# Performance work log

Hardware: AMD Instinct MI355X
Metric: run time of the kernel (lower is better)

## Reference

```python
import jax, jax.numpy as jnp
import numpy as np

N = 50000   # nodes
E = 600000  # edges
H = 128     # hidden_features
TW = 1      # time_window
L = 6       # hidden_layer
MSG_IN = 2 * H + TW + 2 + 1   # 260
UPD_IN = 2 * H + 1            # 257
LX = 1.0; LY = 1.0; TMAX = 1.0; DT = 0.01
EPS = 1e-5


def setup_inputs() -> dict:
    ks = iter(jax.random.split(jax.random.key(0), 64))
    rn = lambda s, sc=0.05: jax.random.normal(next(ks), s, dtype=jnp.float32) * sc
    z = lambda s: jnp.zeros(s, jnp.float32)
    o = lambda s: jnp.ones(s, jnp.float32)
    return {
        'u': rn((N, TW), 1.0),
        'pos': jax.random.uniform(next(ks), (N, 3), dtype=jnp.float32),
        'edge_index': jax.random.randint(next(ks), (2, E), 0, N),
        'emb_W1': rn((TW + 3, H)), 'emb_b1': z((H,)), 'emb_g1': o((H,)), 'emb_be1': z((H,)),
        'emb_W2': rn((H, H)), 'emb_b2': z((H,)), 'emb_g2': o((H,)), 'emb_be2': z((H,)),
        'm1_W': rn((L, MSG_IN, H)), 'm1_b': z((L, H)),
        'm2_W': rn((L, H, H)), 'm2_b': z((L, H)),
        'u1_W': rn((L, UPD_IN, H)), 'u1_b': z((L, H)),
        'u2_W': rn((L, H, H)), 'u2_b': z((L, H)),
        'bn_g': o((L, H)), 'bn_b': z((L, H)),
        'c1_W': rn((4, 1, 16)), 'c1_b': z((4,)),
        'c2_W': rn((8, 4, 12)), 'c2_b': z((8,)),
        'c3_W': rn((1, 8, 8)), 'c3_b': z((1,)),
    }


def _bn(x, g, b):
    # BatchNorm1d, training-mode batch statistics over node dim (biased var)
    mu = jnp.mean(x, 0)
    v = jnp.var(x, 0)
    return g * (x - mu) * jax.lax.rsqrt(v + EPS) + b


def _conv1d(x, W, b, stride):
    y = jax.lax.conv_general_dilated(x, W, (stride,), 'VALID',
                                     dimension_numbers=('NCH', 'OIH', 'NCH'))
    return y + b[None, :, None]


def _forward(u, pos, emb_W1, emb_b1, emb_g1, emb_be1, emb_W2, emb_b2, emb_g2, emb_be2,
             m1_W, m1_b, m2_W, m2_b, u1_W, u1_b, u2_W, u2_b, bn_g, bn_b,
             c1_W, c1_b, c2_W, c2_b, c3_W, c3_b, edge_index):
    px = pos[:, 1:2] / LX
    py = pos[:, 2:3] / LY
    variables = pos[:, 0:1] / TMAX  # pos_t, only eq variable

    # embedding MLP: Linear -> BN -> ReLU -> Linear -> BN
    h = jnp.concatenate([u, px, py, variables], -1) @ emb_W1 + emb_b1
    h = jax.nn.relu(_bn(h, emb_g1, emb_be1))
    h = _bn(h @ emb_W2 + emb_b2, emb_g2, emb_be2)

    src, dst = edge_index[0], edge_index[1]  # x_j = x[src], x_i = x[dst]
    du = u[dst] - u[src]
    dpx = px[dst] - px[src]
    dpy = py[dst] - py[src]
    var_i = variables[dst]
    deg = jax.ops.segment_sum(jnp.ones((E,), jnp.float32), dst, num_segments=N)
    deg = jnp.maximum(deg, 1.0)[:, None]  # mean aggregation denom (0-deg -> 0)

    for i in range(L):
        # message: cat(x_i, x_j, u_i-u_j, dpos_x, dpos_y, variables_i) -> 2xMLP
        msg_in = jnp.concatenate([h[dst], h[src], du, dpx, dpy, var_i], -1)  # [E,260]
        m = jax.nn.relu(msg_in @ m1_W[i] + m1_b[i])
        m = jax.nn.relu(m @ m2_W[i] + m2_b[i])
        agg = jax.ops.segment_sum(m, dst, num_segments=N) / deg  # mean scatter
        # update: cat(x, message, variables) -> 2xMLP, residual, BN
        up = jax.nn.relu(jnp.concatenate([h, agg, variables], -1) @ u1_W[i] + u1_b[i])
        up = jax.nn.relu(up @ u2_W[i] + u2_b[i])
        h = _bn(h + up, bn_g[i], bn_b[i])

    # output CNN over feature dim: [N,1,128] -> [N,1,1]
    x = h[:, None, :]
    x = jax.nn.relu(_conv1d(x, c1_W, c1_b, 3))
    x = jax.nn.relu(_conv1d(x, c2_W, c2_b, 3))
    diff = _conv1d(x, c3_W, c3_b, 2)[:, 0, :]  # [N, TW]

    dt = jnp.cumsum(jnp.full((1, TW), DT * 0.1, dtype=h.dtype), axis=1)
    return dt * diff


def reference(u, pos, edge_index, emb_W1, emb_b1, emb_g1, emb_be1, emb_W2, emb_b2,
              emb_g2, emb_be2, m1_W, m1_b, m2_W, m2_b, u1_W, u1_b, u2_W, u2_b,
              bn_g, bn_b, c1_W, c1_b, c2_W, c2_b, c3_W, c3_b):
    return _forward(u, pos, emb_W1, emb_b1, emb_g1, emb_be1, emb_W2, emb_b2, emb_g2,
                    emb_be2, m1_W, m1_b, m2_W, m2_b, u1_W, u1_b, u2_W, u2_b,
                    bn_g, bn_b, c1_W, c1_b, c2_W, c2_b, c3_W, c3_b, edge_index)
```

## Files before the change

kernel.cpp:

```cpp
#include <hip/hip_runtime.h>

#define NN 50000
#define NE 600000
#define HD 128
#define NL 6
#define DPB 16

typedef __attribute__((ext_vector_type(8))) short bf16x8;
typedef __attribute__((ext_vector_type(4))) float f32x4;

__device__ inline unsigned short f2bf(float x) {
  unsigned u = __float_as_uint(x);
  u += 0x7FFF + ((u >> 16) & 1);
  return (unsigned short)(u >> 16);
}
__device__ inline float bf2f(unsigned short s) {
  return __uint_as_float((unsigned)s << 16);
}
__device__ inline unsigned pk2(float a, float b) {
  return (unsigned)f2bf(a) | ((unsigned)f2bf(b) << 16);
}

__global__ void k_code(float* __restrict__ out, float code) {
  if (threadIdx.x == 0 && blockIdx.x == 0) out[0] = code;
}


__global__ __launch_bounds__(256) void k_w2t(const float* __restrict__ W, unsigned short* __restrict__ T) {
  int idx = blockIdx.x * 256 + threadIdx.x;
  if (idx >= NL * HD * HD) return;
  int l = idx >> 14, r = idx & 16383;
  int n = r >> 7, k = r & 127;
  T[idx] = f2bf(W[(l << 14) + (k << 7) + n]);
}

__global__ __launch_bounds__(256) void k_u1t(const float* __restrict__ W, unsigned short* __restrict__ T) {
  int idx = blockIdx.x * 256 + threadIdx.x;
  if (idx >= NL * 128 * 256) return;
  int l = idx >> 15, r = idx & 32767;
  int n = r >> 8, k = r & 255;
  T[idx] = f2bf(W[l * 32896 + k * 128 + n]);
}

__global__ __launch_bounds__(256) void k_abt(const float* __restrict__ W, unsigned short* __restrict__ T) {
  int idx = blockIdx.x * 256 + threadIdx.x;
  if (idx >= NL * 256 * 128) return;
  int l = idx >> 15, r = idx & 32767;
  int n = r >> 7, k = r & 127;
  int row = (n < 128) ? k : 128 + k;
  int col = n & 127;
  T[idx] = f2bf(W[l * 33280 + row * 128 + col]);
}


__global__ __launch_bounds__(256) void k_deg(const int* __restrict__ ei, int* __restrict__ deg) {
  int e = blockIdx.x * 256 + threadIdx.x;
  if (e < NE) {
    int d = ei[NE + e];
    if (d >= 0 && d < NN) atomicAdd(&deg[d], 1);
  }
}

__global__ __launch_bounds__(256) void k_scan1(const int* __restrict__ deg, int* __restrict__ cursor,
                                               int* __restrict__ blk, float* __restrict__ invd) {
  __shared__ int sd[256];
  int t = threadIdx.x;
  int i = blockIdx.x * 256 + t;
  int v = (i < NN) ? deg[i] : 0;
  sd[t] = v;
  __syncthreads();
  for (int off = 1; off < 256; off <<= 1) {
    int x = (t >= off) ? sd[t - off] : 0;
    __syncthreads();
    if (t >= off) sd[t] += x;
    __syncthreads();
  }
  int incl = sd[t];
  if (i < NN) {
    cursor[i] = incl - v;
    invd[i] = 1.0f / fmaxf((float)v, 1.0f);
  }
  if (t == 255) blk[blockIdx.x] = incl;
}

__global__ __launch_bounds__(256) void k_scan2(int* __restrict__ blk, int nb) {
  __shared__ int sd[256];
  int t = threadIdx.x;
  int v = (t < nb) ? blk[t] : 0;
  sd[t] = v;
  __syncthreads();
  for (int off = 1; off < 256; off <<= 1) {
    int x = (t >= off) ? sd[t - off] : 0;
    __syncthreads();
    if (t >= off) sd[t] += x;
    __syncthreads();
  }
  if (t < nb) blk[t] = sd[t] - v;
}

__global__ __launch_bounds__(256) void k_scan3(int* __restrict__ cursor, const int* __restrict__ blk,
                                               int* __restrict__ rowstart) {
  int i = blockIdx.x * 256 + threadIdx.x;
  if (i < NN) {
    int v = cursor[i] + blk[blockIdx.x];
    cursor[i] = v;
    rowstart[i] = v;
  }
  if (i == 0) rowstart[NN] = NE;
}

__global__ __launch_bounds__(256) void k_scatter(const int* __restrict__ ei, const float* __restrict__ u,
                                                 const float* __restrict__ pos, int* __restrict__ cursor,
                                                 int* __restrict__ ssrc, int* __restrict__ sdst,
                                                 float* __restrict__ sfeat) {
  int e = blockIdx.x * 256 + threadIdx.x;
  if (e >= NE) return;
  int s = ei[e], d = ei[NE + e];
  s = s < 0 ? 0 : (s >= NN ? NN - 1 : s);
  d = d < 0 ? 0 : (d >= NN ? NN - 1 : d);
  int p = atomicAdd(&cursor[d], 1);
  ssrc[p] = s;
  sdst[p] = d;
  float du  = u[d] - u[s];
  float dpx = pos[d*3+1] - pos[s*3+1];
  float dpy = pos[d*3+2] - pos[s*3+2];
  float vi  = pos[d*3+0];
  ((float4*)sfeat)[p] = make_float4(du, dpx, dpy, vi);
}


__global__ __launch_bounds__(256) void k_emb1(const float* __restrict__ u, const float* __restrict__ pos,
                                              const float* __restrict__ W, const float* __restrict__ b,
                                              float* __restrict__ h, double* __restrict__ P) {
  __shared__ float xs[32 * 129];
  int tid = threadIdx.x;
  int nl = tid & 31, jg = tid >> 5;
  int gn = blockIdx.x * 32 + nl;
  float f0 = 0.f, f1 = 0.f, f2 = 0.f, f3 = 0.f;
  if (gn < NN) { f0 = u[gn]; f1 = pos[gn*3+1]; f2 = pos[gn*3+2]; f3 = pos[gn*3+0]; }
  float x[16];
#pragma unroll
  for (int q = 0; q < 4; ++q) {
    int j = (jg << 4) + (q << 2);
    float4 w0 = *(const float4*)(W + 0*HD + j);
    float4 w1 = *(const float4*)(W + 1*HD + j);
    float4 w2 = *(const float4*)(W + 2*HD + j);
    float4 w3 = *(const float4*)(W + 3*HD + j);
    float4 bb = *(const float4*)(b + j);
    x[q*4+0] = f0*w0.x + f1*w1.x + f2*w2.x + f3*w3.x + bb.x;
    x[q*4+1] = f0*w0.y + f1*w1.y + f2*w2.y + f3*w3.y + bb.y;
    x[q*4+2] = f0*w0.z + f1*w1.z + f2*w2.z + f3*w3.z + bb.z;
    x[q*4+3] = f0*w0.w + f1*w1.w + f2*w2.w + f3*w3.w + bb.w;
  }
  if (gn < NN) {
#pragma unroll
    for (int q = 0; q < 4; ++q)
      *(float4*)(h + (size_t)gn*HD + (jg<<4) + (q<<2)) = make_float4(x[q*4+0], x[q*4+1], x[q*4+2], x[q*4+3]);
  }
#pragma unroll
  for (int i = 0; i < 16; ++i) xs[nl*129 + (jg<<4) + i] = (gn < NN) ? x[i] : 0.f;
  __syncthreads();
  if (tid < HD) {
    double s = 0.0, sq = 0.0;
    for (int e = 0; e < 32; ++e) { double v = (double)xs[e*129 + tid]; s += v; sq += v*v; }
    size_t pb = (size_t)blockIdx.x * 256;
    P[pb + tid] = s;
    P[pb + 128 + tid] = sq;
  }
}

__global__ __launch_bounds__(256) void k_emb2(float* __restrict__ h, const float* __restrict__ W,
                                              const float* __restrict__ b, double* __restrict__ P) {
  __shared__ float hs[32 * 129];
  int tid = threadIdx.x;
  int base = blockIdx.x * 32;
#pragma unroll
  for (int r = 0; r < 16; ++r) {
    int lin = r*256 + tid;
    int n = lin >> 7, j = lin & 127;
    int gn = base + n;
    hs[n*129 + j] = (gn < NN) ? h[(size_t)gn*HD + j] : 0.f;
  }
  __syncthreads();
  int nl = tid & 31, jg = tid >> 5;
  int gn = base + nl;
  float acc[16];
#pragma unroll
  for (int q = 0; q < 4; ++q) {
    float4 bb = *(const float4*)(b + (jg<<4) + (q<<2));
    acc[q*4+0] = bb.x; acc[q*4+1] = bb.y; acc[q*4+2] = bb.z; acc[q*4+3] = bb.w;
  }
  for (int k = 0; k < HD; ++k) {
    float a = hs[nl*129 + k];
    const float4* wp = (const float4*)(W + (size_t)k*HD + (jg<<4));
#pragma unroll
    for (int q = 0; q < 4; ++q) {
      float4 wv = wp[q];
      acc[q*4+0] = fmaf(a, wv.x, acc[q*4+0]);
      acc[q*4+1] = fmaf(a, wv.y, acc[q*4+1]);
      acc[q*4+2] = fmaf(a, wv.z, acc[q*4+2]);
      acc[q*4+3] = fmaf(a, wv.w, acc[q*4+3]);
    }
  }
  if (gn < NN) {
#pragma unroll
    for (int q = 0; q < 4; ++q)
      *(float4*)(h + (size_t)gn*HD + (jg<<4) + (q<<2)) = make_float4(acc[q*4+0], acc[q*4+1], acc[q*4+2], acc[q*4+3]);
  }
  __syncthreads();
#pragma unroll
  for (int i = 0; i < 16; ++i) hs[nl*129 + (jg<<4) + i] = (gn < NN) ? acc[i] : 0.f;
  __syncthreads();
  if (tid < HD) {
    double s = 0.0, sq = 0.0;
    for (int e = 0; e < 32; ++e) { double v = (double)hs[e*129 + tid]; s += v; sq += v*v; }
    size_t pb = (size_t)blockIdx.x * 256;
    P[pb + tid] = s;
    P[pb + 128 + tid] = sq;
  }
}

__global__ __launch_bounds__(256) void k_redP(const double* __restrict__ P, int nrows,
                                              float* __restrict__ musig) {
  __shared__ double sd[256];
  __shared__ double sq_[256];
  int c = blockIdx.x;
  int t = threadIdx.x;
  double s = 0.0, q = 0.0;
  for (int k = t; k < nrows; k += 256) {
    s += P[(size_t)k*256 + c];
    q += P[(size_t)k*256 + 128 + c];
  }
  sd[t] = s; sq_[t] = q;
  __syncthreads();
  for (int off = 128; off; off >>= 1) {
    if (t < off) { sd[t] += sd[t + off]; sq_[t] += sq_[t + off]; }
    __syncthreads();
  }
  if (t == 0) {
    double mu  = sd[0] / (double)NN;
    double var = sq_[0] / (double)NN - mu * mu;
    musig[c]      = (float)mu;
    musig[HD + c] = (float)(1.0 / sqrt(var + 1e-5));
  }
}

__global__ void k_redA(const double* __restrict__ stats, float* __restrict__ musig) {
  int c = threadIdx.x;
  double mu  = stats[c] / (double)NN;
  double var = stats[128 + c] / (double)NN - mu * mu;
  musig[c]      = (float)mu;
  musig[HD + c] = (float)(1.0 / sqrt(var + 1e-5));
}

__global__ __launch_bounds__(256) void k_bn(float* __restrict__ h, const float* __restrict__ musig,
                                            const float* __restrict__ g, const float* __restrict__ be,
                                            int relu) {
  int idx = blockIdx.x * 256 + threadIdx.x;
  if (idx >= NN * HD) return;
  int j = idx & 127;
  float x = h[idx];
  x = g[j] * (x - musig[j]) * musig[HD + j] + be[j];
  if (relu) x = fmaxf(x, 0.f);
  h[idx] = x;
}


__global__ __launch_bounds__(256) void k_ab_mfma(float* __restrict__ h,
                                                 const unsigned short* __restrict__ abt,
                                                 const float* __restrict__ musig,
                                                 const float* __restrict__ g, const float* __restrict__ be,
                                                 int applyBN,
                                                 unsigned short* __restrict__ A, unsigned short* __restrict__ B) {
  __shared__ unsigned short hbf[32 * 136];
  int tid = threadIdx.x;
  int base = blockIdx.x * 32;
#pragma unroll
  for (int r = 0; r < 16; ++r) {
    int lin = r*256 + tid;
    int n = lin >> 7, j = lin & 127;
    int gn = base + n;
    float hv = (gn < NN) ? h[(size_t)gn*HD + j] : 0.f;
    if (applyBN) {
      hv = g[j] * (hv - musig[j]) * musig[HD + j] + be[j];
      if (gn < NN) h[(size_t)gn*HD + j] = hv;
    }
    hbf[n*136 + j] = f2bf((gn < NN) ? hv : 0.f);
  }
  __syncthreads();
  int wv = tid >> 6, lane = tid & 63;
  int quad = lane >> 4, mrow = lane & 15;
  int mt = wv & 1, ntg = wv >> 1;
  f32x4 acc[8];
#pragma unroll
  for (int t = 0; t < 8; ++t) acc[t] = (f32x4){0.f,0.f,0.f,0.f};
#pragma unroll
  for (int ks = 0; ks < 4; ++ks) {
    bf16x8 a = *(const bf16x8*)(hbf + (mt*16 + mrow)*136 + ks*32 + quad*8);
#pragma unroll
    for (int t = 0; t < 8; ++t) {
      bf16x8 b = *(const bf16x8*)(abt + (size_t)((ntg*8 + t)*16 + mrow)*128 + ks*32 + quad*8);
      acc[t] = __builtin_amdgcn_mfma_f32_16x16x32_bf16(a, b, acc[t], 0, 0, 0);
    }
  }
#pragma unroll
  for (int t = 0; t < 8; ++t) {
    int c = (ntg*8 + t)*16 + mrow;
#pragma unroll
    for (int r = 0; r < 4; ++r) {
      int gn = base + mt*16 + quad*4 + r;
      if (gn < NN) {
        if (c < 128) A[(size_t)gn*HD + c]       = f2bf(acc[t][r]);
        else         B[(size_t)gn*HD + c - 128] = f2bf(acc[t][r]);
      }
    }
  }
}


__global__ __launch_bounds__(256, 2) void k_msgupd(const unsigned short* __restrict__ A,
                                                   const unsigned short* __restrict__ B,
                                                   const int* __restrict__ ssrc, const int* __restrict__ sdst,
                                                   const float* __restrict__ sfeat, const float* __restrict__ invd,
                                                   const int* __restrict__ rowstart,
                                                   const float* __restrict__ W1, const float* __restrict__ b1,
                                                   const unsigned short* __restrict__ w2t, const float* __restrict__ b2,
                                                   float* __restrict__ h, const float* __restrict__ pos,
                                                   const unsigned short* __restrict__ u1t,
                                                   const float* __restrict__ U1var, const float* __restrict__ ub1,
                                                   const unsigned short* __restrict__ u2t, const float* __restrict__ ub2,
                                                   double* __restrict__ P) {
  __shared__ __align__(16) unsigned short smAB[16*136 + 32*136];
  __shared__ __align__(16) unsigned short smD[128 * 40];
  __shared__ float wes[6 * 128];
  __shared__ int ldstD[64];

  unsigned short* As   = smAB;
  unsigned short* m1bf = smAB + 16*136;
  unsigned short* abf  = smAB;
  unsigned short* m2bf = smD;
  unsigned short* u1bf = smD;

  int tid = threadIdx.x;
  int base = blockIdx.x * DPB;

  {
    int row = tid >> 4, c16 = tid & 15;
    int gn = base + row;
    bf16x8 v = (bf16x8){0,0,0,0,0,0,0,0};
    if (gn < NN) v = *(const bf16x8*)(A + (size_t)gn*HD + c16*8);
    *(bf16x8*)(As + row*136 + c16*8) = v;
  }
  for (int i = tid; i < 768; i += 256) {
    int k = i >> 7, j = i & 127;
    float v;
    if (k < 4)       v = W1[(size_t)(256 + k)*HD + j];
    else if (k == 4) v = b1[j];
    else             v = b2[j];
    wes[i] = v;
  }
  int rs0 = rowstart[base];
  int rs1 = rowstart[base + DPB];
  __syncthreads();

  int wv = tid >> 6, lane = tid & 63;
  int quad = lane >> 4, mrow = lane & 15;
  int mt = wv & 1, ntg = wv >> 1;
  int el = tid & 31, jg = tid >> 5;

  const float4* sf4 = (const float4*)sfeat;
  int nch = (rs1 - rs0 + 31) >> 5;

  f32x4 aggA[4];
#pragma unroll
  for (int t = 0; t < 4; ++t) aggA[t] = (f32x4){0.f,0.f,0.f,0.f};

  int d_c; float4 f_c;
  int s_n1, d_n1; float4 f_n1;
  {
    int e = rs0 + el; bool v = e < rs1;
    int sc = v ? ssrc[e] : 0;
    d_c = v ? (sdst[e] - base) : 999;
    f_c = v ? sf4[e] : make_float4(0.f, 0.f, 0.f, 0.f);
    s_n1 = sc;
  }
  bf16x8 b0_c = *(const bf16x8*)(B + (size_t)s_n1*HD + (jg<<4));
  bf16x8 b1_c = *(const bf16x8*)(B + (size_t)s_n1*HD + (jg<<4) + 8);
  {
    int e = rs0 + 32 + el; bool v = e < rs1;
    s_n1 = v ? ssrc[e] : 0;
    d_n1 = v ? (sdst[e] - base) : 999;
    f_n1 = v ? sf4[e] : make_float4(0.f, 0.f, 0.f, 0.f);
  }

  int par = 0;
  for (int ch = 0; ch < nch; ++ch) {
    int e0 = rs0 + ch*32;
    int s_n2, d_n2; float4 f_n2;
    {
      int e = e0 + 64 + el; bool v = e < rs1;
      s_n2 = v ? ssrc[e] : 0;
      d_n2 = v ? (sdst[e] - base) : 999;
      f_n2 = v ? sf4[e] : make_float4(0.f, 0.f, 0.f, 0.f);
    }
    bf16x8 b0_n = *(const bf16x8*)(B + (size_t)s_n1*HD + (jg<<4));
    bf16x8 b1_n = *(const bf16x8*)(B + (size_t)s_n1*HD + (jg<<4) + 8);

    if (tid < 32) ldstD[par*32 + tid] = d_c;

    {
      int dA = (d_c < DPB) ? d_c : 0;
      float f0 = f_c.x, f1 = f_c.y, f2 = f_c.z, f3 = f_c.w;
      const unsigned short* Ar = As + dA*136 + (jg<<4);
      bf16x8 a0 = *(const bf16x8*)(Ar);
      bf16x8 a1 = *(const bf16x8*)(Ar + 8);
      float m1v[16];
#pragma unroll
      for (int q = 0; q < 4; ++q) {
        float4 w0 = *(const float4*)(wes + 0*128 + (jg<<4) + (q<<2));
        float4 w1 = *(const float4*)(wes + 1*128 + (jg<<4) + (q<<2));
        float4 w2 = *(const float4*)(wes + 2*128 + (jg<<4) + (q<<2));
        float4 w3 = *(const float4*)(wes + 3*128 + (jg<<4) + (q<<2));
        float4 bb = *(const float4*)(wes + 4*128 + (jg<<4) + (q<<2));
#pragma unroll
        for (int z = 0; z < 4; ++z) {
          int i = q*4 + z;
          unsigned short avs = (i < 8) ? (unsigned short)a0[i] : (unsigned short)a1[i-8];
          unsigned short bvs = (i < 8) ? (unsigned short)b0_c[i] : (unsigned short)b1_c[i-8];
          float we  = (z==0?w0.x:(z==1?w0.y:(z==2?w0.z:w0.w)));
          float w1e = (z==0?w1.x:(z==1?w1.y:(z==2?w1.z:w1.w)));
          float w2e = (z==0?w2.x:(z==1?w2.y:(z==2?w2.z:w2.w)));
          float w3e = (z==0?w3.x:(z==1?w3.y:(z==2?w3.z:w3.w)));
          float bbe = (z==0?bb.x:(z==1?bb.y:(z==2?bb.z:bb.w)));
          m1v[i] = fmaxf(bf2f(avs) + bf2f(bvs) + f0*we + f1*w1e + f2*w2e + f3*w3e + bbe, 0.f);
        }
      }
      unsigned* pp = (unsigned*)(m1bf + el*136 + (jg<<4));
#pragma unroll
      for (int i = 0; i < 8; ++i)
        pp[i] = pk2(m1v[2*i], m1v[2*i+1]);
    }
    __syncthreads();

    {
      f32x4 acc0 = (f32x4){0.f,0.f,0.f,0.f}, acc1 = acc0, acc2 = acc0, acc3 = acc0;
#pragma unroll
      for (int ks = 0; ks < 4; ++ks) {
        bf16x8 a = *(const bf16x8*)(m1bf + (mt*16 + mrow)*136 + ks*32 + quad*8);
        bf16x8 bf0 = *(const bf16x8*)(w2t + ((ntg*4+0)*16 + mrow)*128 + ks*32 + quad*8);
        bf16x8 bf1 = *(const bf16x8*)(w2t + ((ntg*4+1)*16 + mrow)*128 + ks*32 + quad*8);
        bf16x8 bf2 = *(const bf16x8*)(w2t + ((ntg*4+2)*16 + mrow)*128 + ks*32 + quad*8);
        bf16x8 bf3 = *(const bf16x8*)(w2t + ((ntg*4+3)*16 + mrow)*128 + ks*32 + quad*8);
        acc0 = __builtin_amdgcn_mfma_f32_16x16x32_bf16(a, bf0, acc0, 0, 0, 0);
        acc1 = __builtin_amdgcn_mfma_f32_16x16x32_bf16(a, bf1, acc1, 0, 0, 0);
        acc2 = __builtin_amdgcn_mfma_f32_16x16x32_bf16(a, bf2, acc2, 0, 0, 0);
        acc3 = __builtin_amdgcn_mfma_f32_16x16x32_bf16(a, bf3, acc3, 0, 0, 0);
      }
      f32x4 av4[4] = {acc0, acc1, acc2, acc3};
      int ebase = mt*16 + quad*4;
#pragma unroll
      for (int t = 0; t < 4; ++t) {
        int c = (ntg*4 + t)*16 + mrow;
        float bb = wes[5*128 + c];
        unsigned q0 = pk2(fmaxf(av4[t][0] + bb, 0.f), fmaxf(av4[t][1] + bb, 0.f));
        unsigned q1 = pk2(fmaxf(av4[t][2] + bb, 0.f), fmaxf(av4[t][3] + bb, 0.f));
        unsigned* mp = (unsigned*)(m2bf + c*40 + ebase);
        mp[0] = q0; mp[1] = q1;
      }
    }
    __syncthreads();

    {
      int myrow = mt*16 + mrow;
      bf16x8 sel;
#pragma unroll
      for (int i = 0; i < 8; ++i) {
        int dl = ldstD[par*32 + quad*8 + i];
        sel[i] = (short)((dl == myrow) ? 0x3F80 : 0);
      }
      bf16x8 p0 = *(const bf16x8*)(m2bf + ((ntg*4+0)*16 + mrow)*40 + quad*8);
      bf16x8 p1 = *(const bf16x8*)(m2bf + ((ntg*4+1)*16 + mrow)*40 + quad*8);
      bf16x8 p2 = *(const bf16x8*)(m2bf + ((ntg*4+2)*16 + mrow)*40 + quad*8);
      bf16x8 p3 = *(const bf16x8*)(m2bf + ((ntg*4+3)*16 + mrow)*40 + quad*8);
      aggA[0] = __builtin_amdgcn_mfma_f32_16x16x32_bf16(sel, p0, aggA[0], 0, 0, 0);
      aggA[1] = __builtin_amdgcn_mfma_f32_16x16x32_bf16(sel, p1, aggA[1], 0, 0, 0);
      aggA[2] = __builtin_amdgcn_mfma_f32_16x16x32_bf16(sel, p2, aggA[2], 0, 0, 0);
      aggA[3] = __builtin_amdgcn_mfma_f32_16x16x32_bf16(sel, p3, aggA[3], 0, 0, 0);
    }

    d_c = d_n1; f_c = f_n1;
    s_n1 = s_n2; d_n1 = d_n2; f_n1 = f_n2;
    b0_c = b0_n; b1_c = b1_n;
    par ^= 1;
  }

  {
    int row = tid >> 4, c16 = tid & 15;
    int gn = base + row;
    float4 h0 = *(const float4*)(h + (size_t)gn*HD + c16*8);
    float4 h1 = *(const float4*)(h + (size_t)gn*HD + c16*8 + 4);
    unsigned* q = (unsigned*)(abf + row*264 + c16*8);
    q[0] = pk2(h0.x, h0.y); q[1] = pk2(h0.z, h0.w);
    q[2] = pk2(h1.x, h1.y); q[3] = pk2(h1.z, h1.w);
  }
  if (mt == 0) {
    float invdv[4];
#pragma unroll
    for (int r = 0; r < 4; ++r) invdv[r] = invd[base + quad*4 + r];
#pragma unroll
    for (int t = 0; t < 4; ++t) {
      int c = (ntg*4 + t)*16 + mrow;
#pragma unroll
      for (int r = 0; r < 4; ++r)
        abf[(quad*4 + r)*264 + 128 + c] = f2bf(aggA[t][r] * invdv[r]);
    }
  }
  __syncthreads();

  int lo = mrow;
  float ub1c[2], uvarc[2], ub2c[2];
#pragma unroll
  for (int t = 0; t < 2; ++t) {
    int c = (wv*2 + t)*16 + lo;
    ub1c[t] = ub1[c]; uvarc[t] = U1var[c]; ub2c[t] = ub2[c];
  }
  float lvarv[4];
#pragma unroll
  for (int r = 0; r < 4; ++r) lvarv[r] = pos[(size_t)(base + quad*4 + r)*3 + 0];

  f32x4 ua[2];
  ua[0] = (f32x4){0.f,0.f,0.f,0.f}; ua[1] = ua[0];
#pragma unroll
  for (int ks = 0; ks < 8; ++ks) {
    bf16x8 a = *(const bf16x8*)(abf + lo*264 + ks*32 + quad*8);
#pragma unroll
    for (int t = 0; t < 2; ++t) {
      bf16x8 b = *(const bf16x8*)(u1t + (size_t)((wv*2 + t)*16 + lo)*256 + ks*32 + quad*8);
      ua[t] = __builtin_amdgcn_mfma_f32_16x16x32_bf16(a, b, ua[t], 0, 0, 0);
    }
  }
#pragma unroll
  for (int t = 0; t < 2; ++t) {
    int c = (wv*2 + t)*16 + lo;
#pragma unroll
    for (int r = 0; r < 4; ++r) {
      float v = fmaxf(ua[t][r] + ub1c[t] + lvarv[r]*uvarc[t], 0.f);
      u1bf[(quad*4 + r)*136 + c] = f2bf(v);
    }
  }
  __syncthreads();

  f32x4 va[2];
  va[0] = (f32x4){0.f,0.f,0.f,0.f}; va[1] = va[0];
#pragma unroll
  for (int ks = 0; ks < 4; ++ks) {
    bf16x8 a = *(const bf16x8*)(u1bf + lo*136 + ks*32 + quad*8);
#pragma unroll
    for (int t = 0; t < 2; ++t) {
      bf16x8 b = *(const bf16x8*)(u2t + (size_t)((wv*2 + t)*16 + lo)*128 + ks*32 + quad*8);
      va[t] = __builtin_amdgcn_mfma_f32_16x16x32_bf16(a, b, va[t], 0, 0, 0);
    }
  }

#pragma unroll
  for (int t = 0; t < 2; ++t) {
    int c = (wv*2 + t)*16 + lo;
    float s = 0.f, q = 0.f;
#pragma unroll
    for (int r = 0; r < 4; ++r) {
      int gn = base + quad*4 + r;
      float x = h[(size_t)gn*HD + c] + fmaxf(va[t][r] + ub2c[t], 0.f);
      h[(size_t)gn*HD + c] = x;
      s += x; q += x*x;
    }
    s += __shfl_xor(s, 16); q += __shfl_xor(q, 16);
    s += __shfl_xor(s, 32); q += __shfl_xor(q, 32);
    if (quad == 0) {
      size_t pb = (size_t)blockIdx.x * 256;
      P[pb + c]       = (double)s;
      P[pb + 128 + c] = (double)q;
    }
  }
}


__global__ __launch_bounds__(256) void k_msg_direct(const float* __restrict__ h,
                                                    const int* __restrict__ ei, const float* __restrict__ u,
                                                    const float* __restrict__ pos, const float* __restrict__ invd,
                                                    const float* __restrict__ W1, const float* __restrict__ b1,
                                                    const float* __restrict__ W2, const float* __restrict__ b2,
                                                    float* __restrict__ agg) {
  __shared__ float hd[32 * 129];
  __shared__ float hsr[32 * 129];
  __shared__ float m1s[32 * 129];
  __shared__ int lsrc[32];
  __shared__ int ldst[32];
  __shared__ float lf[32][4];
  int tid = threadIdx.x;
  int base = blockIdx.x * 32;
  if (tid < 32) {
    int e = base + tid;
    int s = ei[e], d = ei[NE + e];
    s = s < 0 ? 0 : (s >= NN ? NN - 1 : s);
    d = d < 0 ? 0 : (d >= NN ? NN - 1 : d);
    lsrc[tid] = s; ldst[tid] = d;
    lf[tid][0] = u[d] - u[s];
    lf[tid][1] = pos[d*3+1] - pos[s*3+1];
    lf[tid][2] = pos[d*3+2] - pos[s*3+2];
    lf[tid][3] = pos[d*3+0];
  }
  __syncthreads();
#pragma unroll
  for (int r = 0; r < 16; ++r) {
    int lin = r*256 + tid;
    int n = lin >> 7, j = lin & 127;
    hd[n*129 + j]  = h[(size_t)ldst[n]*HD + j];
    hsr[n*129 + j] = h[(size_t)lsrc[n]*HD + j];
  }
  __syncthreads();
  int el = tid & 31, jg = tid >> 5;
  float f0 = lf[el][0], f1 = lf[el][1], f2 = lf[el][2], f3 = lf[el][3];
  const float* We = W1 + 256*HD + (jg<<4);
  float acc[16];
#pragma unroll
  for (int q = 0; q < 4; ++q) {
    float4 w0 = *(const float4*)(We + 0*HD + (q<<2));
    float4 w1 = *(const float4*)(We + 1*HD + (q<<2));
    float4 w2 = *(const float4*)(We + 2*HD + (q<<2));
    float4 w3 = *(const float4*)(We + 3*HD + (q<<2));
    float4 bb = *(const float4*)(b1 + (jg<<4) + (q<<2));
    acc[q*4+0] = f0*w0.x + f1*w1.x + f2*w2.x + f3*w3.x + bb.x;
    acc[q*4+1] = f0*w0.y + f1*w1.y + f2*w2.y + f3*w3.y + bb.y;
    acc[q*4+2] = f0*w0.z + f1*w1.z + f2*w2.z + f3*w3.z + bb.z;
    acc[q*4+3] = f0*w0.w + f1*w1.w + f2*w2.w + f3*w3.w + bb.w;
  }
  for (int k = 0; k < HD; ++k) {
    float a  = hd[el*129 + k];
    float bs = hsr[el*129 + k];
    const float4* wa = (const float4*)(W1 + (size_t)k*HD + (jg<<4));
    const float4* wb = (const float4*)(W1 + (size_t)(128 + k)*HD + (jg<<4));
#pragma unroll
    for (int q = 0; q < 4; ++q) {
      float4 w1v = wa[q];
      float4 w2v = wb[q];
      acc[q*4+0] = fmaf(a, w1v.x, fmaf(bs, w2v.x, acc[q*4+0]));
      acc[q*4+1] = fmaf(a, w1v.y, fmaf(bs, w2v.y, acc[q*4+1]));
      acc[q*4+2] = fmaf(a, w1v.z, fmaf(bs, w2v.z, acc[q*4+2]));
      acc[q*4+3] = fmaf(a, w1v.w, fmaf(bs, w2v.w, acc[q*4+3]));
    }
  }
#pragma unroll
  for (int i = 0; i < 16; ++i) m1s[el*129 + (jg<<4) + i] = fmaxf(acc[i], 0.f);
  __syncthreads();
  float acc2[16];
#pragma unroll
  for (int q = 0; q < 4; ++q) {
    float4 bb = *(const float4*)(b2 + (jg<<4) + (q<<2));
    acc2[q*4+0] = bb.x; acc2[q*4+1] = bb.y; acc2[q*4+2] = bb.z; acc2[q*4+3] = bb.w;
  }
  for (int k = 0; k < HD; ++k) {
    float a = m1s[el*129 + k];
    const float4* wp = (const float4*)(W2 + (size_t)k*HD + (jg<<4));
#pragma unroll
    for (int q = 0; q < 4; ++q) {
      float4 wv = wp[q];
      acc2[q*4+0] = fmaf(a, wv.x, acc2[q*4+0]);
      acc2[q*4+1] = fmaf(a, wv.y, acc2[q*4+1]);
      acc2[q*4+2] = fmaf(a, wv.z, acc2[q*4+2]);
      acc2[q*4+3] = fmaf(a, wv.w, acc2[q*4+3]);
    }
  }
#pragma unroll
  for (int i = 0; i < 16; ++i) hd[el*129 + (jg<<4) + i] = fmaxf(acc2[i], 0.f);
  __syncthreads();
  if (tid < HD) {
    int j = tid;
    for (int e = 0; e < 32; ++e) {
      int de = ldst[e];
      atomicAdd(&agg[(size_t)de*HD + j], hd[e*129 + j] * invd[de]);
    }
  }
}


__global__ __launch_bounds__(256) void k_upd(float* __restrict__ h, const float* __restrict__ agg,
                                             const float* __restrict__ pos,
                                             const float* __restrict__ W1, const float* __restrict__ b1,
                                             const float* __restrict__ W2, const float* __restrict__ b2,
                                             double* __restrict__ stats) {
  __shared__ float hs[32 * 129];
  __shared__ float as_[32 * 129];
  int tid = threadIdx.x;
  int base = blockIdx.x * 32;
#pragma unroll
  for (int r = 0; r < 16; ++r) {
    int lin = r*256 + tid;
    int n = lin >> 7, j = lin & 127;
    int gn = base + n;
    hs[n*129 + j]  = (gn < NN) ? h[(size_t)gn*HD + j]   : 0.f;
    as_[n*129 + j] = (gn < NN) ? agg[(size_t)gn*HD + j] : 0.f;
  }
  __syncthreads();
  int nl = tid & 31, jg = tid >> 5;
  int gn = base + nl;
  float var = (gn < NN) ? pos[gn*3+0] : 0.f;
  float acc[16];
#pragma unroll
  for (int q = 0; q < 4; ++q) {
    int j = (jg<<4) + (q<<2);
    float4 bb = *(const float4*)(b1 + j);
    float4 wv = *(const float4*)(W1 + 256*HD + j);
    acc[q*4+0] = fmaf(var, wv.x, bb.x);
    acc[q*4+1] = fmaf(var, wv.y, bb.y);
    acc[q*4+2] = fmaf(var, wv.z, bb.z);
    acc[q*4+3] = fmaf(var, wv.w, bb.w);
  }
  for (int k = 0; k < HD; ++k) {
    float a = hs[nl*129 + k];
    float g = as_[nl*129 + k];
    const float4* w1p = (const float4*)(W1 + (size_t)k*HD + (jg<<4));
    const float4* w2p = (const float4*)(W1 + (size_t)(128 + k)*HD + (jg<<4));
#pragma unroll
    for (int q = 0; q < 4; ++q) {
      float4 wa = w1p[q];
      float4 wb = w2p[q];
      acc[q*4+0] = fmaf(a, wa.x, fmaf(g, wb.x, acc[q*4+0]));
      acc[q*4+1] = fmaf(a, wa.y, fmaf(g, wb.y, acc[q*4+1]));
      acc[q*4+2] = fmaf(a, wa.z, fmaf(g, wb.z, acc[q*4+2]));
      acc[q*4+3] = fmaf(a, wa.w, fmaf(g, wb.w, acc[q*4+3]));
    }
  }
  float up1[16];
#pragma unroll
  for (int i = 0; i < 16; ++i) up1[i] = fmaxf(acc[i], 0.f);
  __syncthreads();
#pragma unroll
  for (int i = 0; i < 16; ++i) as_[nl*129 + (jg<<4) + i] = up1[i];
  __syncthreads();
  float acc2[16];
#pragma unroll
  for (int q = 0; q < 4; ++q) {
    float4 bb = *(const float4*)(b2 + (jg<<4) + (q<<2));
    acc2[q*4+0] = bb.x; acc2[q*4+1] = bb.y; acc2[q*4+2] = bb.z; acc2[q*4+3] = bb.w;
  }
  for (int k = 0; k < HD; ++k) {
    float a = as_[nl*129 + k];
    const float4* wp = (const float4*)(W2 + (size_t)k*HD + (jg<<4));
#pragma unroll
    for (int q = 0; q < 4; ++q) {
      float4 wv = wp[q];
      acc2[q*4+0] = fmaf(a, wv.x, acc2[q*4+0]);
      acc2[q*4+1] = fmaf(a, wv.y, acc2[q*4+1]);
      acc2[q*4+2] = fmaf(a, wv.z, acc2[q*4+2]);
      acc2[q*4+3] = fmaf(a, wv.w, acc2[q*4+3]);
    }
  }
  float x[16];
#pragma unroll
  for (int i = 0; i < 16; ++i)
    x[i] = hs[nl*129 + (jg<<4) + i] + fmaxf(acc2[i], 0.f);
  if (gn < NN) {
#pragma unroll
    for (int q = 0; q < 4; ++q)
      *(float4*)(h + (size_t)gn*HD + (jg<<4) + (q<<2)) = make_float4(x[q*4+0], x[q*4+1], x[q*4+2], x[q*4+3]);
  }
  __syncthreads();
#pragma unroll
  for (int i = 0; i < 16; ++i) hs[nl*129 + (jg<<4) + i] = (gn < NN) ? x[i] : 0.f;
  __syncthreads();
  if (tid < HD) {
    double s = 0.0, sq = 0.0;
    for (int e = 0; e < 32; ++e) { double v = (double)hs[e*129 + tid]; s += v; sq += v*v; }
    atomicAdd(&stats[tid], s);
    atomicAdd(&stats[HD + tid], sq);
  }
}


__global__ __launch_bounds__(256) void k_conv(const float* __restrict__ h,
                                              const float* __restrict__ musig,
                                              const float* __restrict__ g, const float* __restrict__ be,
                                              int applyBN,
                                              const float* __restrict__ c1W, const float* __restrict__ c1b,
                                              const float* __restrict__ c2W, const float* __restrict__ c2b,
                                              const float* __restrict__ c3W, const float* __restrict__ c3b,
                                              float* __restrict__ out) {
  __shared__ float xs[4][128];
  __shared__ float o1[4][152];
  __shared__ float o2[4][72];
  int tid = threadIdx.x;
  int w = tid >> 6, lane = tid & 63;
  int n = blockIdx.x * 4 + w;
#pragma unroll
  for (int half = 0; half < 2; ++half) {
    int j = half * 64 + lane;
    float v = h[(size_t)n*HD + j];
    if (applyBN) v = g[j] * (v - musig[j]) * musig[HD + j] + be[j];
    xs[w][j] = v;
  }
  __syncthreads();
  for (int o = lane; o < 152; o += 64) {
    int oc = o / 38, t = o % 38;
    float s = c1b[oc];
#pragma unroll
    for (int k = 0; k < 16; ++k) s = fmaf(xs[w][t*3 + k], c1W[oc*16 + k], s);
    o1[w][oc*38 + t] = fmaxf(s, 0.f);
  }
  __syncthreads();
  for (int o = lane; o < 72; o += 64) {
    int oc = o / 9, t = o % 9;
    float s = c2b[oc];
    for (int ic = 0; ic < 4; ++ic) {
#pragma unroll
      for (int k = 0; k < 12; ++k) s = fmaf(o1[w][ic*38 + t*3 + k], c2W[oc*48 + ic*12 + k], s);
    }
    o2[w][oc*9 + t] = fmaxf(s, 0.f);
  }
  __syncthreads();
  int ic = lane >> 3, k = lane & 7;
  float t3 = o2[w][ic*9 + k] * c3W[ic*8 + k];
  for (int off = 32; off; off >>= 1) t3 += __shfl_down(t3, off);
  if (lane == 0) out[n] = 0.001f * (t3 + c3b[0]);
}


extern "C" void kernel_launch(void* const* d_in, const int* in_sizes, int n_in,
                              void* d_out, int out_size, void* d_ws, size_t ws_size,
                              hipStream_t stream) {
  (void)out_size;
  float* out = (float*)d_out;

  static const int expect[27] = {
    50000, 150000, 1200000,
    512, 128, 128, 128,
    16384, 128, 128, 128,
    199680, 768, 98304, 768, 197376, 768, 98304, 768,
    768, 768,
    64, 4, 384, 8, 64, 1
  };
  if (n_in != 27) { k_code<<<1, 64, 0, stream>>>(out, 5000099.f); return; }
  for (int i = 0; i < 27; ++i)
    if (in_sizes[i] != expect[i]) { k_code<<<1, 64, 0, stream>>>(out, 5000100.f + (float)i); return; }

  const float* u    = (const float*)d_in[0];
  const float* pos  = (const float*)d_in[1];
  const int*   ei   = (const int*)d_in[2];
  const float* eW1  = (const float*)d_in[3];
  const float* eb1  = (const float*)d_in[4];
  const float* eg1  = (const float*)d_in[5];
  const float* ebe1 = (const float*)d_in[6];
  const float* eW2  = (const float*)d_in[7];
  const float* eb2  = (const float*)d_in[8];
  const float* eg2  = (const float*)d_in[9];
  const float* ebe2 = (const float*)d_in[10];
  const float* m1W  = (const float*)d_in[11];
  const float* m1b  = (const float*)d_in[12];
  const float* m2W  = (const float*)d_in[13];
  const float* m2b  = (const float*)d_in[14];
  const float* u1W  = (const float*)d_in[15];
  const float* u1b  = (const float*)d_in[16];
  const float* u2W  = (const float*)d_in[17];
  const float* u2b  = (const float*)d_in[18];
  const float* bng  = (const float*)d_in[19];
  const float* bnb  = (const float*)d_in[20];
  const float* c1W  = (const float*)d_in[21];
  const float* c1b  = (const float*)d_in[22];
  const float* c2W  = (const float*)d_in[23];
  const float* c2b  = (const float*)d_in[24];
  const float* c3W  = (const float*)d_in[25];
  const float* c3b  = (const float*)d_in[26];

  char* wsp = (char*)d_ws;
  size_t off = 0;
  auto alloc = [&](size_t bytes) -> void* {
    void* p = wsp + off;
    off = (off + bytes + 255) & ~(size_t)255;
    return p;
  };
  double* stats  = (double*)alloc(256 * 8);
  float*  musig  = (float*)alloc(256 * 4);
  int*    deg    = (int*)alloc((size_t)NN * 4);
  int*    cursor = (int*)alloc((size_t)NN * 4);
  int*    blk    = (int*)alloc(256 * 4);
  float*  invd   = (float*)alloc((size_t)NN * 4);
  float*  h      = (float*)alloc((size_t)NN * HD * 4);
  float*  agg    = (float*)alloc((size_t)NN * HD * 4);
  double* P      = (double*)alloc((size_t)3200 * 256 * 8);
  size_t needed_direct = off;
  unsigned short* A = (unsigned short*)alloc((size_t)NN * HD * 2);
  unsigned short* B = (unsigned short*)alloc((size_t)NN * HD * 2);
  float*  sfeat  = (float*)alloc((size_t)NE * 4 * 4);
  int*    ssrc   = (int*)alloc((size_t)NE * 4);
  int*    sdst   = (int*)alloc((size_t)NE * 4);
  int*    rowstart = (int*)alloc((size_t)(NN + 1) * 4);
  unsigned short* w2t = (unsigned short*)alloc((size_t)NL * HD * HD * 2);
  unsigned short* u2t = (unsigned short*)alloc((size_t)NL * HD * HD * 2);
  unsigned short* u1t = (unsigned short*)alloc((size_t)NL * HD * 256 * 2);
  unsigned short* abt = (unsigned short*)alloc((size_t)NL * 256 * HD * 2);
  size_t needed_fast = off;

  if (ws_size < needed_direct) {
    k_code<<<1, 64, 0, stream>>>(out, (float)(9000000u + (unsigned)(ws_size >> 20)));
    return;
  }
  const bool fast = (ws_size >= needed_fast);

  const int nbN  = (NN + 255) / 256;
  const int nbE  = (NE + 255) / 256;
  const int nt32 = (NN + 31) / 32;
  const int nbBN = NN * HD / 256;
  const int nbMU = NN / DPB;

  hipMemsetAsync(deg, 0, (size_t)NN * 4, stream);
  k_deg<<<nbE, 256, 0, stream>>>(ei, deg);
  k_scan1<<<nbN, 256, 0, stream>>>(deg, cursor, blk, invd);
  if (fast) {
    k_scan2<<<1, 256, 0, stream>>>(blk, nbN);
    k_scan3<<<nbN, 256, 0, stream>>>(cursor, blk, rowstart);
    k_scatter<<<nbE, 256, 0, stream>>>(ei, u, pos, cursor, ssrc, sdst, sfeat);
    k_w2t<<<(NL*HD*HD + 255) / 256, 256, 0, stream>>>(m2W, w2t);
    k_w2t<<<(NL*HD*HD + 255) / 256, 256, 0, stream>>>(u2W, u2t);
    k_u1t<<<(NL*HD*256 + 255) / 256, 256, 0, stream>>>(u1W, u1t);
    k_abt<<<(NL*256*HD + 255) / 256, 256, 0, stream>>>(m1W, abt);
  }

  k_emb1<<<nt32, 256, 0, stream>>>(u, pos, eW1, eb1, h, P);
  k_redP<<<128, 256, 0, stream>>>(P, nt32, musig);
  k_bn<<<nbBN, 256, 0, stream>>>(h, musig, eg1, ebe1, 1);
  k_emb2<<<nt32, 256, 0, stream>>>(h, eW2, eb2, P);
  k_redP<<<128, 256, 0, stream>>>(P, nt32, musig);
  k_bn<<<nbBN, 256, 0, stream>>>(h, musig, eg2, ebe2, 0);

  for (int i = 0; i < NL; ++i) {
    if (fast) {
      k_ab_mfma<<<nt32, 256, 0, stream>>>(h, abt + (size_t)i * 256 * HD,
                                          musig, bng + (size_t)(i > 0 ? i - 1 : 0) * HD,
                                          bnb + (size_t)(i > 0 ? i - 1 : 0) * HD,
                                          (i > 0) ? 1 : 0, A, B);
      k_msgupd<<<nbMU, 256, 0, stream>>>(A, B, ssrc, sdst, sfeat, invd, rowstart,
                                         m1W + (size_t)i * 260 * HD, m1b + (size_t)i * HD,
                                         w2t + (size_t)i * HD * HD, m2b + (size_t)i * HD,
                                         h, pos,
                                         u1t + (size_t)i * HD * 256,
                                         u1W + (size_t)i * 32896 + 256 * HD,
                                         u1b + (size_t)i * HD,
                                         u2t + (size_t)i * HD * HD,
                                         u2b + (size_t)i * HD, P);
      k_redP<<<128, 256, 0, stream>>>(P, nbMU, musig);
    } else {
      hipMemsetAsync(agg, 0, (size_t)NN * HD * 4, stream);
      k_msg_direct<<<NE / 32, 256, 0, stream>>>(h, ei, u, pos, invd,
                                                m1W + (size_t)i * 260 * HD, m1b + (size_t)i * HD,
                                                m2W + (size_t)i * HD * HD, m2b + (size_t)i * HD, agg);
      hipMemsetAsync(stats, 0, 256 * 8, stream);
      k_upd<<<nt32, 256, 0, stream>>>(h, agg, pos,
                                      u1W + (size_t)i * 257 * HD, u1b + (size_t)i * HD,
                                      u2W + (size_t)i * HD * HD, u2b + (size_t)i * HD, stats);
      k_redA<<<1, 128, 0, stream>>>(stats, musig);
      k_bn<<<nbBN, 256, 0, stream>>>(h, musig, bng + (size_t)i * HD, bnb + (size_t)i * HD, 0);
    }
  }

  k_conv<<<NN / 4, 256, 0, stream>>>(h, musig, bng + (size_t)(NL - 1) * HD, bnb + (size_t)(NL - 1) * HD,
                                     fast ? 1 : 0,
                                     c1W, c1b, c2W, c2b, c3W, c3b, out);
}
```

Before: 1.707 ms.

## Keep message GEMM output in registers and aggregate via lane shuffles

The message-MLP second layer now tiles work so each wave computes both 16-edge row tiles for two column tiles. The ReLU'd bf16 results are shuffled across lanes directly into the B-operand layout of the selection MFMA, instead of going through a shared-memory transpose buffer. This removes one __syncthreads and the m2 LDS round trip per edge chunk, and double-buffers the m1 staging area so the next chunk's writes do not race the current reads. It adds many cross-lane shuffles per chunk, and the LDS footprint and aliasing of u1bf change.

```diff
diff --git a/kernel.cpp b/kernel.cpp
--- a/kernel.cpp
+++ b/kernel.cpp
@@ -330,16 +330,14 @@
                                                    const float* __restrict__ U1var, const float* __restrict__ ub1,
                                                    const unsigned short* __restrict__ u2t, const float* __restrict__ ub2,
                                                    double* __restrict__ P) {
-  __shared__ __align__(16) unsigned short smAB[16*136 + 32*136];
-  __shared__ __align__(16) unsigned short smD[128 * 40];
+  __shared__ __align__(16) unsigned short smAB[16*136 + 2*32*136];
   __shared__ float wes[6 * 128];
   __shared__ int ldstD[64];
 
   unsigned short* As   = smAB;
-  unsigned short* m1bf = smAB + 16*136;
+  unsigned short* m1b0 = smAB + 16*136;
   unsigned short* abf  = smAB;
-  unsigned short* m2bf = smD;
-  unsigned short* u1bf = smD;
+  unsigned short* u1bf = smAB + 16*264;
 
   int tid = threadIdx.x;
   int base = blockIdx.x * DPB;
@@ -365,15 +363,17 @@
 
   int wv = tid >> 6, lane = tid & 63;
   int quad = lane >> 4, mrow = lane & 15;
-  int mt = wv & 1, ntg = wv >> 1;
   int el = tid & 31, jg = tid >> 5;
+
+  float b2c[2];
+#pragma unroll
+  for (int t = 0; t < 2; ++t) b2c[t] = wes[5*128 + (wv*2 + t)*16 + mrow];
 
   const float4* sf4 = (const float4*)sfeat;
   int nch = (rs1 - rs0 + 31) >> 5;
 
-  f32x4 aggA[4];
-#pragma unroll
-  for (int t = 0; t < 4; ++t) aggA[t] = (f32x4){0.f,0.f,0.f,0.f};
+  f32x4 agg[2];
+  agg[0] = (f32x4){0.f,0.f,0.f,0.f}; agg[1] = agg[0];
 
   int d_c; float4 f_c;
   int s_n1, d_n1; float4 f_n1;
@@ -407,6 +407,7 @@
     bf16x8 b1_n = *(const bf16x8*)(B + (size_t)s_n1*HD + (jg<<4) + 8);
 
     if (tid < 32) ldstD[par*32 + tid] = d_c;
+    unsigned short* m1bf = m1b0 + par*32*136;
 
     {
       int dA = (d_c < DPB) ? d_c : 0;
@@ -443,49 +444,54 @@
     __syncthreads();
 
     {
-      f32x4 acc0 = (f32x4){0.f,0.f,0.f,0.f}, acc1 = acc0, acc2 = acc0, acc3 = acc0;
+      f32x4 acc[2][2];
+      acc[0][0] = (f32x4){0.f,0.f,0.f,0.f}; acc[0][1] = acc[0][0];
+      acc[1][0] = acc[0][0]; acc[1][1] = acc[0][0];
 #pragma unroll
       for (int ks = 0; ks < 4; ++ks) {
-        bf16x8 a = *(const bf16x8*)(m1bf + (mt*16 + mrow)*136 + ks*32 + quad*8);
-        bf16x8 bf0 = *(const bf16x8*)(w2t + ((ntg*4+0)*16 + mrow)*128 + ks*32 + quad*8);
-        bf16x8 bf1 = *(const bf16x8*)(w2t + ((ntg*4+1)*16 + mrow)*128 + ks*32 + quad*8);
-        bf16x8 bf2 = *(const bf16x8*)(w2t + ((ntg*4+2)*16 + mrow)*128 + ks*32 + quad*8);
-        bf16x8 bf3 = *(const bf16x8*)(w2t + ((ntg*4+3)*16 + mrow)*128 + ks*32 + quad*8);
-        acc0 = __builtin_amdgcn_mfma_f32_16x16x32_bf16(a, bf0, acc0, 0, 0, 0);
-        acc1 = __builtin_amdgcn_mfma_f32_16x16x32_bf16(a, bf1, acc1, 0, 0, 0);
-        acc2 = __builtin_amdgcn_mfma_f32_16x16x32_bf16(a, bf2, acc2, 0, 0, 0);
-        acc3 = __builtin_amdgcn_mfma_f32_16x16x32_bf16(a, bf3, acc3, 0, 0, 0);
+        bf16x8 a0 = *(const bf16x8*)(m1bf + (mrow)*136      + ks*32 + quad*8);
+        bf16x8 a1 = *(const bf16x8*)(m1bf + (16 + mrow)*136 + ks*32 + quad*8);
+#pragma unroll
+        for (int t = 0; t < 2; ++t) {
+          bf16x8 b = *(const bf16x8*)(w2t + (size_t)((wv*2 + t)*16 + mrow)*128 + ks*32 + quad*8);
+          acc[0][t] = __builtin_amdgcn_mfma_f32_16x16x32_bf16(a0, b, acc[0][t], 0, 0, 0);
+          acc[1][t] = __builtin_amdgcn_mfma_f32_16x16x32_bf16(a1, b, acc[1][t], 0, 0, 0);
+        }
       }
-      f32x4 av4[4] = {acc0, acc1, acc2, acc3};
-      int ebase = mt*16 + quad*4;
-#pragma unroll
-      for (int t = 0; t < 4; ++t) {
-        int c = (ntg*4 + t)*16 + mrow;
-        float bb = wes[5*128 + c];
-        unsigned q0 = pk2(fmaxf(av4[t][0] + bb, 0.f), fmaxf(av4[t][1] + bb, 0.f));
-        unsigned q1 = pk2(fmaxf(av4[t][2] + bb, 0.f), fmaxf(av4[t][3] + bb, 0.f));
-        unsigned* mp = (unsigned*)(m2bf + c*40 + ebase);
-        mp[0] = q0; mp[1] = q1;
-      }
-    }
-    __syncthreads();
-
-    {
-      int myrow = mt*16 + mrow;
+
       bf16x8 sel;
 #pragma unroll
       for (int i = 0; i < 8; ++i) {
         int dl = ldstD[par*32 + quad*8 + i];
-        sel[i] = (short)((dl == myrow) ? 0x3F80 : 0);
+        sel[i] = (short)((dl == mrow) ? 0x3F80 : 0);
       }
-      bf16x8 p0 = *(const bf16x8*)(m2bf + ((ntg*4+0)*16 + mrow)*40 + quad*8);
-      bf16x8 p1 = *(const bf16x8*)(m2bf + ((ntg*4+1)*16 + mrow)*40 + quad*8);
-      bf16x8 p2 = *(const bf16x8*)(m2bf + ((ntg*4+2)*16 + mrow)*40 + quad*8);
-      bf16x8 p3 = *(const bf16x8*)(m2bf + ((ntg*4+3)*16 + mrow)*40 + quad*8);
-      aggA[0] = __builtin_amdgcn_mfma_f32_16x16x32_bf16(sel, p0, aggA[0], 0, 0, 0);
-      aggA[1] = __builtin_amdgcn_mfma_f32_16x16x32_bf16(sel, p1, aggA[1], 0, 0, 0);
-      aggA[2] = __builtin_amdgcn_mfma_f32_16x16x32_bf16(sel, p2, aggA[2], 0, 0, 0);
-      aggA[3] = __builtin_amdgcn_mfma_f32_16x16x32_bf16(sel, p3, aggA[3], 0, 0, 0);
+
+      int src0 = ((quad & 1) * 2) * 16 + mrow;
+      int src1 = src0 + 16;
+      bool useE0 = (quad < 2);
+#pragma unroll
+      for (int t = 0; t < 2; ++t) {
+        float bb = b2c[t];
+        unsigned p00 = pk2(fmaxf(acc[0][t][0] + bb, 0.f), fmaxf(acc[0][t][1] + bb, 0.f));
+        unsigned p01 = pk2(fmaxf(acc[0][t][2] + bb, 0.f), fmaxf(acc[0][t][3] + bb, 0.f));
+        unsigned p10 = pk2(fmaxf(acc[1][t][0] + bb, 0.f), fmaxf(acc[1][t][1] + bb, 0.f));
+        unsigned p11 = pk2(fmaxf(acc[1][t][2] + bb, 0.f), fmaxf(acc[1][t][3] + bb, 0.f));
+        unsigned a00 = (unsigned)__shfl((int)p00, src0);
+        unsigned a01 = (unsigned)__shfl((int)p01, src0);
+        unsigned a02 = (unsigned)__shfl((int)p00, src1);
+        unsigned a03 = (unsigned)__shfl((int)p01, src1);
+        unsigned e10 = (unsigned)__shfl((int)p10, src0);
+        unsigned e11 = (unsigned)__shfl((int)p11, src0);
+        unsigned e12 = (unsigned)__shfl((int)p10, src1);
+        unsigned e13 = (unsigned)__shfl((int)p11, src1);
+        bf16x8 bfr;
+        unsigned* bp = (unsigned*)&bfr;
+        bp[0] = useE0 ? a00 : e10;
+        bp[1] = useE0 ? a01 : e11;
+        bp[2] = useE0 ? a02 : e12;
+        bp[3] = useE0 ? a03 : e13;
+        agg[t] = __builtin_amdgcn_mfma_f32_16x16x32_bf16(sel, bfr, agg[t], 0, 0, 0);
+      }
     }
 
     d_c = d_n1; f_c = f_n1;
@@ -493,6 +499,7 @@
     b0_c = b0_n; b1_c = b1_n;
     par ^= 1;
   }
+  __syncthreads();
 
   {
     int row = tid >> 4, c16 = tid & 15;
@@ -503,16 +510,16 @@
     q[0] = pk2(h0.x, h0.y); q[1] = pk2(h0.z, h0.w);
     q[2] = pk2(h1.x, h1.y); q[3] = pk2(h1.z, h1.w);
   }
-  if (mt == 0) {
+  {
     float invdv[4];
 #pragma unroll
     for (int r = 0; r < 4; ++r) invdv[r] = invd[base + quad*4 + r];
 #pragma unroll
-    for (int t = 0; t < 4; ++t) {
-      int c = (ntg*4 + t)*16 + mrow;
+    for (int t = 0; t < 2; ++t) {
+      int c = (wv*2 + t)*16 + mrow;
 #pragma unroll
       for (int r = 0; r < 4; ++r)
-        abf[(quad*4 + r)*264 + 128 + c] = f2bf(aggA[t][r] * invdv[r]);
+        abf[(quad*4 + r)*264 + 128 + c] = f2bf(agg[t][r] * invdv[r]);
     }
   }
   __syncthreads();
```

Result: faster. 1.498 ms, median of 2 (-12.2%).
